# Kernel optimization log

Measured on AMD Instinct MI355X. Metric: run time of the kernel, lower is better.

## Reference

```python
import jax, jax.numpy as jnp
import numpy as np

N_NODES = 100000
N_EDGES = 3200000
N_GRAPHS = 256
HID = 128


def _glorot(key, shape):
    fan_in = shape[1]
    return jax.random.normal(key, shape, dtype=jnp.float32) / jnp.sqrt(jnp.float32(fan_in))


def setup_inputs() -> dict:
    key = jax.random.key(0)
    ks = jax.random.split(key, 16)
    x = jax.random.normal(ks[0], (N_NODES, 50), dtype=jnp.float32)
    edge_index = jax.random.randint(ks[1], (2, N_EDGES), 0, N_NODES, dtype=jnp.int32)
    batch = jnp.sort(jax.random.randint(ks[2], (N_NODES,), 0, N_GRAPHS, dtype=jnp.int32))
    d1, d2, d3 = HID, HID * 2, HID * 4
    params = {
        'w1l': _glorot(ks[3], (d1, 50)), 'b1': jnp.zeros((d1,), jnp.float32), 'w1r': _glorot(ks[4], (d1, 50)),
        'w2l': _glorot(ks[5], (d2, d1)), 'b2': jnp.zeros((d2,), jnp.float32), 'w2r': _glorot(ks[6], (d2, d1)),
        'w3l': _glorot(ks[7], (d3, d2)), 'b3': jnp.zeros((d3,), jnp.float32), 'w3r': _glorot(ks[8], (d3, d2)),
        'fc1_w': _glorot(ks[9], (d2, d3)), 'fc1_b': jnp.zeros((d2,), jnp.float32),
        'fc2_w': _glorot(ks[10], (d1, d2)), 'fc2_b': jnp.zeros((d1,), jnp.float32),
        'cls_w': _glorot(ks[11], (15, d1)), 'cls_b': jnp.zeros((15,), jnp.float32),
    }
    return {'x': x, 'edge_index': edge_index, 'batch': batch, **params}


def _sage_conv(x, src, dst, wl, b, wr):
    # PyG SAGEConv (mean aggr): out = lin_l(mean_j x_j) + lin_r(x_i)
    agg = jax.ops.segment_sum(x[src], dst, num_segments=N_NODES)
    deg = jax.ops.segment_sum(jnp.ones((src.shape[0],), x.dtype), dst, num_segments=N_NODES)
    agg = agg / jnp.maximum(deg, 1.0)[:, None]
    return agg @ wl.T + b + x @ wr.T


def reference(x, edge_index, batch,
              w1l, b1, w1r, w2l, b2, w2r, w3l, b3, w3r,
              fc1_w, fc1_b, fc2_w, fc2_b, cls_w, cls_b):
    src, dst = edge_index[0], edge_index[1]
    # eval mode: dropout is identity
    h = jax.nn.leaky_relu(_sage_conv(x, src, dst, w1l, b1, w1r), negative_slope=0.01)
    h = jax.nn.relu(_sage_conv(h, src, dst, w2l, b2, w2r))
    h = jax.nn.relu(_sage_conv(h, src, dst, w3l, b3, w3r))
    # global mean pool over graphs
    pooled = jax.ops.segment_sum(h, batch, num_segments=N_GRAPHS)
    cnt = jax.ops.segment_sum(jnp.ones((h.shape[0],), h.dtype), batch, num_segments=N_GRAPHS)
    pooled = pooled / jnp.maximum(cnt, 1.0)[:, None]
    z = jax.nn.relu(pooled @ fc1_w.T + fc1_b)
    z = jax.nn.relu(z @ fc2_w.T + fc2_b)
    return z @ cls_w.T + cls_b
```

## Files before the change

kernel.cpp:

```cpp
#include <hip/hip_runtime.h>
#include <hip/hip_bf16.h>

#define N_NODES 100000
#define N_EDGES 3200000
#define N_GRAPHS 256
#define CAP 80

typedef __hip_bfloat16 bf16;
using f32x4  = __attribute__((ext_vector_type(4))) float;
using f32x2  = __attribute__((ext_vector_type(2))) float;
using short8 = __attribute__((ext_vector_type(8))) short;

__global__ void rank_kernel(const int* __restrict__ dst, int* __restrict__ cnt,
                            unsigned short* __restrict__ rank) {
    int e = blockIdx.x * blockDim.x + threadIdx.x;
    if (e < N_EDGES) rank[e] = (unsigned short)atomicAdd(&cnt[dst[e]], 1);
}

__global__ void place_slot_kernel(const int* __restrict__ src, const int* __restrict__ dst,
                                  const unsigned short* __restrict__ rank,
                                  int* __restrict__ cols) {
    int e = blockIdx.x * blockDim.x + threadIdx.x;
    if (e < N_EDGES) {
        int r = rank[e];
        if (r < CAP) cols[dst[e] * CAP + r] = src[e];
    }
}

__global__ void invdeg_kernel(const int* __restrict__ cnt, float* __restrict__ invdeg) {
    int n = blockIdx.x * blockDim.x + threadIdx.x;
    if (n < N_NODES) invdeg[n] = 1.0f / fmaxf((float)cnt[n], 1.0f);
}

__global__ void xprep_kernel(const float* __restrict__ x, bf16* __restrict__ xb) {
    int t = blockIdx.x * blockDim.x + threadIdx.x;
    if (t >= N_NODES * 64) return;
    int n = t >> 6, f = t & 63;
    xb[t] = __float2bfloat16(f < 50 ? x[(size_t)n * 50 + f] : 0.f);
}

__device__ __forceinline__ void wcvt(const float* __restrict__ s, bf16* __restrict__ d,
                                     int Din, int Kp, int lt) {
    int o = lt / Kp, kk = lt % Kp;
    d[lt] = __float2bfloat16(kk < Din ? s[(size_t)o * Din + kk] : 0.f);
}

__global__ void wprep_all_kernel(const float* w1l, const float* w1r,
                                 const float* w2l, const float* w2r,
                                 const float* w3l, const float* w3r,
                                 bf16* w1l_b, bf16* w1r_b, bf16* w2l_b, bf16* w2r_b,
                                 bf16* w3l_b, bf16* w3r_b) {
    int t = blockIdx.x * blockDim.x + threadIdx.x;
    if      (t < 8192)   wcvt(w1l, w1l_b, 50, 64, t);
    else if (t < 16384)  wcvt(w1r, w1r_b, 50, 64, t - 8192);
    else if (t < 49152)  wcvt(w2l, w2l_b, 128, 128, t - 16384);
    else if (t < 81920)  wcvt(w2r, w2r_b, 128, 128, t - 49152);
    else if (t < 212992) wcvt(w3l, w3l_b, 256, 256, t - 81920);
    else if (t < 344064) wcvt(w3r, w3r_b, 256, 256, t - 212992);
}

template <int D>
__global__ void aggv_kernel(const bf16* __restrict__ h, const int* __restrict__ cnt,
                            const int* __restrict__ cols, const float* __restrict__ invdeg,
                            bf16* __restrict__ AG) {
    constexpr int L = D / 8;
    int n = blockIdx.x * (256 / L) + threadIdx.x / L;
    int lane = threadIdx.x % L;
    if (n >= N_NODES) return;
    const int* cp = cols + (size_t)n * CAP;
    int deg = min(cnt[n], CAP);
    float acc[8] = {};
    auto accum = [&](uint4 v) {
        const unsigned short* u = (const unsigned short*)&v;
#pragma unroll
        for (int i = 0; i < 8; ++i) {
            union { unsigned int ui; float f; } cv;
            cv.ui = ((unsigned int)u[i]) << 16;
            acc[i] += cv.f;
        }
    };
    int j = 0;
    for (; j + 4 <= deg; j += 4) {
        int c0 = cp[j], c1 = cp[j + 1], c2 = cp[j + 2], c3 = cp[j + 3];
        uint4 v0 = *(const uint4*)&h[(size_t)c0 * D + lane * 8];
        uint4 v1 = *(const uint4*)&h[(size_t)c1 * D + lane * 8];
        uint4 v2 = *(const uint4*)&h[(size_t)c2 * D + lane * 8];
        uint4 v3 = *(const uint4*)&h[(size_t)c3 * D + lane * 8];
        accum(v0); accum(v1); accum(v2); accum(v3);
    }
    for (; j < deg; ++j) accum(*(const uint4*)&h[(size_t)cp[j] * D + lane * 8]);
    float inv = invdeg[n];
    union { uint4 u; bf16 h8[8]; } o;
#pragma unroll
    for (int i = 0; i < 8; ++i) o.h8[i] = __float2bfloat16(acc[i] * inv);
    *(uint4*)&AG[(size_t)n * D + lane * 8] = o.u;
}

template <int D>
__global__ void aggv8_kernel(const unsigned char* __restrict__ h8,
                             const int* __restrict__ cnt,
                             const int* __restrict__ cols, const float* __restrict__ invdeg,
                             bf16* __restrict__ AG) {
    constexpr int L = D / 8;
    int n = blockIdx.x * (256 / L) + threadIdx.x / L;
    int lane = threadIdx.x % L;
    if (n >= N_NODES) return;
    const int* cp = cols + (size_t)n * CAP;
    int deg = min(cnt[n], CAP);
    float acc[8] = {};
    auto accum = [&](uint2 v) {
        f32x2 a0 = __builtin_amdgcn_cvt_pk_f32_fp8(v.x, false);
        f32x2 a1 = __builtin_amdgcn_cvt_pk_f32_fp8(v.x, true);
        f32x2 a2 = __builtin_amdgcn_cvt_pk_f32_fp8(v.y, false);
        f32x2 a3 = __builtin_amdgcn_cvt_pk_f32_fp8(v.y, true);
        acc[0] += a0[0]; acc[1] += a0[1]; acc[2] += a1[0]; acc[3] += a1[1];
        acc[4] += a2[0]; acc[5] += a2[1]; acc[6] += a3[0]; acc[7] += a3[1];
    };
    int j = 0;
    for (; j + 8 <= deg; j += 8) {
        uint2 v[8];
#pragma unroll
        for (int q = 0; q < 8; ++q)
            v[q] = *(const uint2*)&h8[(size_t)cp[j + q] * D + lane * 8];
#pragma unroll
        for (int q = 0; q < 8; ++q) accum(v[q]);
    }
    for (; j < deg; ++j) accum(*(const uint2*)&h8[(size_t)cp[j] * D + lane * 8]);
    float inv = invdeg[n];
    union { uint4 u; bf16 hb[8]; } o;
#pragma unroll
    for (int i = 0; i < 8; ++i) o.hb[i] = __float2bfloat16(acc[i] * inv);
    *(uint4*)&AG[(size_t)n * D + lane * 8] = o.u;
}

template <int ACT, int POOL, int OUT8>
__global__ __launch_bounds__(256) void glds_gemm(
        const bf16* __restrict__ A1, const bf16* __restrict__ A2, int Kh,
        const bf16* __restrict__ B1, const bf16* __restrict__ B2,
        const float* __restrict__ bias, bf16* __restrict__ out,
        unsigned char* __restrict__ out8,
        int M, int Dout,
        const int* __restrict__ batch, float* __restrict__ pooled) {
    __shared__ alignas(16) bf16 As[2][128][32];
    __shared__ alignas(16) bf16 Bs[2][128][32];
    __shared__ int sbatch[128];

    const int tid = threadIdx.x;
    const int n0 = blockIdx.y * 128;
    const int o0 = blockIdx.x * 128;

    if (POOL && tid < 128) {
        int n = n0 + tid;
        sbatch[tid] = (n < M) ? batch[n] : -1;
    }

    const int lane = tid & 63;
    const int w = tid >> 6;
    const int wr = w >> 1, wc = w & 1;
    const int lr = lane & 15, hi = lane >> 4;
    const int l4 = lane >> 2;
    const int kc8 = (lane & 3) * 8;

    f32x4 acc[4][4] = {};

    auto stage = [&](int buf, int k0) {
        const bf16* Ap;
        const bf16* Bp;
        int kk;
        if (k0 < Kh) { Ap = A1; Bp = B1; kk = k0; }
        else         { Ap = A2; Bp = B2; kk = k0 - Kh; }
#pragma unroll
        for (int c = 0; c < 2; ++c) {
            int rl = w * 32 + c * 16 + l4;
            size_t ga = (size_t)min(n0 + rl, M - 1) * (size_t)Kh + kk + kc8;
            __builtin_amdgcn_global_load_lds(
                (const __attribute__((address_space(1))) void*)(Ap + ga),
                (__attribute__((address_space(3))) void*)&As[buf][w * 32 + c * 16][0], 16, 0, 0);
            size_t gb = (size_t)(o0 + rl) * (size_t)Kh + kk + kc8;
            __builtin_amdgcn_global_load_lds(
                (const __attribute__((address_space(1))) void*)(Bp + gb),
                (__attribute__((address_space(3))) void*)&Bs[buf][w * 32 + c * 16][0], 16, 0, 0);
        }
    };

    const int nt = (2 * Kh) / 32;
    stage(0, 0);
    asm volatile("s_waitcnt vmcnt(0)\n\ts_barrier" ::: "memory");

    int cur = 0;
    for (int t = 0; t < nt; ++t) {
        if (t + 1 < nt) stage(cur ^ 1, (t + 1) * 32);

        short8 af[4], bfr[4];
#pragma unroll
        for (int m = 0; m < 4; ++m)
            af[m] = *(const short8*)&As[cur][wr * 64 + m * 16 + lr][hi * 8];
#pragma unroll
        for (int n = 0; n < 4; ++n)
            bfr[n] = *(const short8*)&Bs[cur][wc * 64 + n * 16 + lr][hi * 8];
#pragma unroll
        for (int m = 0; m < 4; ++m)
#pragma unroll
            for (int n = 0; n < 4; ++n)
                acc[m][n] = __builtin_amdgcn_mfma_f32_16x16x32_bf16(af[m], bfr[n], acc[m][n], 0, 0, 0);

        if (t + 1 < nt)
            asm volatile("s_waitcnt vmcnt(0)\n\ts_barrier" ::: "memory");
        cur ^= 1;
    }

    float bias_v[4];
#pragma unroll
    for (int n = 0; n < 4; ++n) bias_v[n] = bias[o0 + wc * 64 + n * 16 + lr];

    if (!POOL) {
#pragma unroll
        for (int m = 0; m < 4; ++m) {
#pragma unroll
            for (int j = 0; j < 4; ++j) {
                int row = n0 + wr * 64 + m * 16 + hi * 4 + j;
                if (row < M) {
#pragma unroll
                    for (int n = 0; n < 4; ++n) {
                        int col = o0 + wc * 64 + n * 16 + lr;
                        float s = acc[m][n][j] + bias_v[n];
                        if (ACT == 0) s = (s >= 0.f) ? s : 0.01f * s;
                        else          s = fmaxf(s, 0.f);
                        out[(size_t)row * Dout + col] = __float2bfloat16(s);
                        if (OUT8) {
                            int p = __builtin_amdgcn_cvt_pk_fp8_f32(s, s, 0, false);
                            out8[(size_t)row * Dout + col] = (unsigned char)(p & 0xff);
                        }
                    }
                }
            }
        }
    } else {
        int lastv = min(127, M - 1 - n0);
        int gmin = sbatch[0], gmax = sbatch[lastv];
        for (int g = gmin; g <= gmax; ++g) {
            float s[4] = {0.f, 0.f, 0.f, 0.f};
#pragma unroll
            for (int m = 0; m < 4; ++m) {
#pragma unroll
                for (int j = 0; j < 4; ++j) {
                    int rl = wr * 64 + m * 16 + hi * 4 + j;
                    if (sbatch[rl] == g) {
#pragma unroll
                        for (int n = 0; n < 4; ++n)
                            s[n] += fmaxf(acc[m][n][j] + bias_v[n], 0.f);
                    }
                }
            }
#pragma unroll
            for (int n = 0; n < 4; ++n) {
                float v = s[n];
                v += __shfl_xor(v, 16, 64);
                v += __shfl_xor(v, 32, 64);
                if (hi == 0)
                    atomicAdd(&pooled[(size_t)g * 512 + o0 + wc * 64 + n * 16 + lr], v);
            }
        }
    }
}

__global__ void bounds_kernel(const int* __restrict__ batch, int* __restrict__ gstart) {
    int g = blockIdx.x * blockDim.x + threadIdx.x;
    if (g > N_GRAPHS) return;
    int lo = 0, hi = N_NODES;
    while (lo < hi) {
        int mid = (lo + hi) >> 1;
        if (batch[mid] < g) lo = mid + 1;
        else hi = mid;
    }
    gstart[g] = lo;
}

__global__ void pool_finalize(float* __restrict__ pooled, const int* __restrict__ gstart) {
    int g = blockIdx.x;
    int f = threadIdx.x;
    float cnt = fmaxf((float)(gstart[g + 1] - gstart[g]), 1.0f);
    pooled[(size_t)g * 512 + f] /= cnt;
}

template <int ACT>
__global__ void mlp_kernel(const float* __restrict__ in, const float* __restrict__ w,
                           const float* __restrict__ b, float* __restrict__ out,
                           int M, int K, int O) {
    int t = blockIdx.x * blockDim.x + threadIdx.x;
    if (t >= M * O) return;
    int m = t / O, o = t % O;
    const float* ip = in + (size_t)m * K;
    const float* wp = w + (size_t)o * K;
    float s = 0.f;
    for (int k = 0; k < K; ++k) s += ip[k] * wp[k];
    s += b[o];
    if (ACT) s = fmaxf(s, 0.f);
    out[(size_t)m * O + o] = s;
}

extern "C" void kernel_launch(void* const* d_in, const int* in_sizes, int n_in,
                              void* d_out, int out_size, void* d_ws, size_t ws_size,
                              hipStream_t stream) {
    const float* x     = (const float*)d_in[0];
    const int*   ei    = (const int*)d_in[1];
    const int*   batch = (const int*)d_in[2];
    const float* w1l = (const float*)d_in[3];
    const float* b1  = (const float*)d_in[4];
    const float* w1r = (const float*)d_in[5];
    const float* w2l = (const float*)d_in[6];
    const float* b2  = (const float*)d_in[7];
    const float* w2r = (const float*)d_in[8];
    const float* w3l = (const float*)d_in[9];
    const float* b3  = (const float*)d_in[10];
    const float* w3r = (const float*)d_in[11];
    const float* fc1_w = (const float*)d_in[12];
    const float* fc1_b = (const float*)d_in[13];
    const float* fc2_w = (const float*)d_in[14];
    const float* fc2_b = (const float*)d_in[15];
    const float* cls_w = (const float*)d_in[16];
    const float* cls_b = (const float*)d_in[17];
    float* out = (float*)d_out;

    const int* src = ei;
    const int* dst = ei + N_EDGES;

    char* wsp = (char*)d_ws;
    size_t used = 0;
    auto alloc = [&](size_t bytes) {
        char* p = wsp + used;
        used += (bytes + 255) & ~(size_t)255;
        return p;
    };
    int*   cnt    = (int*)alloc((size_t)N_NODES * 4);
    int*   cols   = (int*)alloc((size_t)N_NODES * CAP * 4);
    float* invdeg = (float*)alloc((size_t)N_NODES * 4);
    int*   gstart = (int*)alloc((size_t)(N_GRAPHS + 1) * 4);
    bf16*  xb     = (bf16*)alloc((size_t)N_NODES * 64 * 2);
    char*  R      = alloc((size_t)N_NODES * 256 * 2);
    bf16*  AG     = (bf16*)R;
    bf16*  h1     = (bf16*)(R + (size_t)N_NODES * 128 * 2);
    bf16*  h2     = (bf16*)alloc((size_t)N_NODES * 256 * 2);
    unsigned short* rank = (unsigned short*)h2;
    unsigned char* h1_8 = (unsigned char*)alloc((size_t)N_NODES * 128);
    unsigned char* h2_8 = (unsigned char*)alloc((size_t)N_NODES * 256);
    bf16*  w1l_b  = (bf16*)alloc(128 * 64 * 2);
    bf16*  w1r_b  = (bf16*)alloc(128 * 64 * 2);
    bf16*  w2l_b  = (bf16*)alloc(256 * 128 * 2);
    bf16*  w2r_b  = (bf16*)alloc(256 * 128 * 2);
    bf16*  w3l_b  = (bf16*)alloc(512 * 256 * 2);
    bf16*  w3r_b  = (bf16*)alloc(512 * 256 * 2);
    float* pooled = (float*)alloc((size_t)N_GRAPHS * 512 * 4);
    float* z1     = (float*)alloc((size_t)N_GRAPHS * 256 * 4);
    float* z2     = (float*)alloc((size_t)N_GRAPHS * 128 * 4);

    if (ws_size < used) return;

    hipMemsetAsync(cnt, 0, (size_t)N_NODES * 4, stream);
    rank_kernel<<<(N_EDGES + 255) / 256, 256, 0, stream>>>(dst, cnt, rank);
    place_slot_kernel<<<(N_EDGES + 255) / 256, 256, 0, stream>>>(src, dst, rank, cols);
    invdeg_kernel<<<(N_NODES + 255) / 256, 256, 0, stream>>>(cnt, invdeg);
    bounds_kernel<<<2, 160, 0, stream>>>(batch, gstart);

    xprep_kernel<<<(N_NODES * 64 + 255) / 256, 256, 0, stream>>>(x, xb);
    wprep_all_kernel<<<(344064 + 255) / 256, 256, 0, stream>>>(
        w1l, w1r, w2l, w2r, w3l, w3r, w1l_b, w1r_b, w2l_b, w2r_b, w3l_b, w3r_b);

    const int MB = (N_NODES + 127) / 128;

    aggv_kernel<64><<<(N_NODES * 8 + 255) / 256, 256, 0, stream>>>(xb, cnt, cols, invdeg, AG);
    glds_gemm<0, 0, 1><<<dim3(1, MB), 256, 0, stream>>>(
        AG, xb, 64, w1l_b, w1r_b, b1, h1, h1_8, N_NODES, 128, nullptr, nullptr);

    aggv8_kernel<128><<<(N_NODES * 16 + 255) / 256, 256, 0, stream>>>(
        h1_8, cnt, cols, invdeg, AG);
    glds_gemm<1, 0, 1><<<dim3(2, MB), 256, 0, stream>>>(
        AG, h1, 128, w2l_b, w2r_b, b2, h2, h2_8, N_NODES, 256, nullptr, nullptr);

    aggv8_kernel<256><<<(N_NODES * 32 + 255) / 256, 256, 0, stream>>>(
        h2_8, cnt, cols, invdeg, AG);
    hipMemsetAsync(pooled, 0, (size_t)N_GRAPHS * 512 * 4, stream);
    glds_gemm<1, 1, 0><<<dim3(4, MB), 256, 0, stream>>>(
        AG, h2, 256, w3l_b, w3r_b, b3, nullptr, nullptr, N_NODES, 512, batch, pooled);
    pool_finalize<<<N_GRAPHS, 512, 0, stream>>>(pooled, gstart);

    mlp_kernel<1><<<(N_GRAPHS * 256 + 255) / 256, 256, 0, stream>>>(
        pooled, fc1_w, fc1_b, z1, N_GRAPHS, 512, 256);
    mlp_kernel<1><<<(N_GRAPHS * 128 + 255) / 256, 256, 0, stream>>>(
        z1, fc2_w, fc2_b, z2, N_GRAPHS, 256, 128);
    mlp_kernel<0><<<(N_GRAPHS * 15 + 255) / 256, 256, 0, stream>>>(
        z2, cls_w, cls_b, out, N_GRAPHS, 128, 15);
}
```

Baseline: 698.7 us.

## Build padded adjacency via two-level bucket sort with shared-memory atomics

Replaces the global-atomic rank/place graph build with a multi-pass bucketed counting sort. Edges are histogrammed by 64-node bucket in shared memory, prefix-scanned, scattered into a packed edge buffer, and then placed into per-node slots with shared-memory atomics. The aim is to remove 3.2M contended global atomics and the random scattered writes, and to fuse the invdeg computation. In exchange it adds six kernel launches, a serial single-block scan, and reuses the h1_8 and h2 buffers as scratch.

```diff
diff --git a/kernel.cpp b/kernel.cpp
--- a/kernel.cpp
+++ b/kernel.cpp
@@ -5,31 +5,125 @@
 #define N_EDGES 3200000
 #define N_GRAPHS 256
 #define CAP 80
+#define NB 1563
+#define NPB 64
+#define PBLK 512
+#define EPB 6250
 
 typedef __hip_bfloat16 bf16;
 using f32x4  = __attribute__((ext_vector_type(4))) float;
 using f32x2  = __attribute__((ext_vector_type(2))) float;
 using short8 = __attribute__((ext_vector_type(8))) short;
 
-__global__ void rank_kernel(const int* __restrict__ dst, int* __restrict__ cnt,
-                            unsigned short* __restrict__ rank) {
-    int e = blockIdx.x * blockDim.x + threadIdx.x;
-    if (e < N_EDGES) rank[e] = (unsigned short)atomicAdd(&cnt[dst[e]], 1);
-}
-
-__global__ void place_slot_kernel(const int* __restrict__ src, const int* __restrict__ dst,
-                                  const unsigned short* __restrict__ rank,
-                                  int* __restrict__ cols) {
-    int e = blockIdx.x * blockDim.x + threadIdx.x;
-    if (e < N_EDGES) {
-        int r = rank[e];
-        if (r < CAP) cols[dst[e] * CAP + r] = src[e];
-    }
-}
-
-__global__ void invdeg_kernel(const int* __restrict__ cnt, float* __restrict__ invdeg) {
-    int n = blockIdx.x * blockDim.x + threadIdx.x;
-    if (n < N_NODES) invdeg[n] = 1.0f / fmaxf((float)cnt[n], 1.0f);
+__global__ __launch_bounds__(256) void p1_count(const int* __restrict__ dst,
+                                                int* __restrict__ bcount) {
+    __shared__ int hist[NB];
+    int i = blockIdx.x;
+    for (int b = threadIdx.x; b < NB; b += 256) hist[b] = 0;
+    __syncthreads();
+    int base = i * EPB;
+    for (int j = threadIdx.x; j < EPB; j += 256)
+        atomicAdd(&hist[dst[base + j] >> 6], 1);
+    __syncthreads();
+    for (int b = threadIdx.x; b < NB; b += 256) bcount[(size_t)b * PBLK + i] = hist[b];
+}
+
+__global__ __launch_bounds__(512) void p2a_total(const int* __restrict__ bcount,
+                                                 int* __restrict__ btotal) {
+    __shared__ int red[512];
+    int b = blockIdx.x;
+    red[threadIdx.x] = bcount[(size_t)b * PBLK + threadIdx.x];
+    __syncthreads();
+    for (int off = 256; off > 0; off >>= 1) {
+        if (threadIdx.x < off) red[threadIdx.x] += red[threadIdx.x + off];
+        __syncthreads();
+    }
+    if (threadIdx.x == 0) btotal[b] = red[0];
+}
+
+__global__ __launch_bounds__(1024) void p2b_scan(const int* __restrict__ btotal,
+                                                 int* __restrict__ bbase) {
+    __shared__ int buf[1024];
+    __shared__ int carry;
+    if (threadIdx.x == 0) carry = 0;
+    __syncthreads();
+    for (int t = 0; t < NB; t += 1024) {
+        int i = t + threadIdx.x;
+        int v = (i < NB) ? btotal[i] : 0;
+        buf[threadIdx.x] = v;
+        __syncthreads();
+        for (int off = 1; off < 1024; off <<= 1) {
+            int tv = (threadIdx.x >= off) ? buf[threadIdx.x - off] : 0;
+            __syncthreads();
+            buf[threadIdx.x] += tv;
+            __syncthreads();
+        }
+        if (i < NB) bbase[i] = carry + buf[threadIdx.x] - v;
+        __syncthreads();
+        if (threadIdx.x == 0) carry += buf[1023];
+        __syncthreads();
+    }
+    if (threadIdx.x == 0) bbase[NB] = carry;
+}
+
+__global__ __launch_bounds__(512) void p2c_off(const int* __restrict__ bcount,
+                                               const int* __restrict__ bbase,
+                                               int* __restrict__ off) {
+    __shared__ int buf[512];
+    int b = blockIdx.x;
+    int v = bcount[(size_t)b * PBLK + threadIdx.x];
+    buf[threadIdx.x] = v;
+    __syncthreads();
+    for (int o = 1; o < 512; o <<= 1) {
+        int t = (threadIdx.x >= o) ? buf[threadIdx.x - o] : 0;
+        __syncthreads();
+        buf[threadIdx.x] += t;
+        __syncthreads();
+    }
+    off[(size_t)threadIdx.x * NB + b] = bbase[b] + buf[threadIdx.x] - v;
+}
+
+__global__ __launch_bounds__(256) void p3_scatter(const int* __restrict__ src,
+                                                  const int* __restrict__ dst,
+                                                  const int* __restrict__ off,
+                                                  unsigned int* __restrict__ ebuf) {
+    __shared__ int loff[NB];
+    int i = blockIdx.x;
+    for (int b = threadIdx.x; b < NB; b += 256) loff[b] = off[(size_t)i * NB + b];
+    __syncthreads();
+    int base = i * EPB;
+    for (int j = threadIdx.x; j < EPB; j += 256) {
+        int d = dst[base + j];
+        int p = atomicAdd(&loff[d >> 6], 1);
+        ebuf[p] = ((unsigned)src[base + j] << 6) | (unsigned)(d & 63);
+    }
+}
+
+__global__ __launch_bounds__(256) void p4_csr(const unsigned int* __restrict__ ebuf,
+                                              const int* __restrict__ bbase,
+                                              int* __restrict__ cols, int* __restrict__ cnt,
+                                              float* __restrict__ invdeg) {
+    __shared__ int lcnt[NPB];
+    int b = blockIdx.x;
+    if (threadIdx.x < NPB) lcnt[threadIdx.x] = 0;
+    __syncthreads();
+    int s = bbase[b], e = bbase[b + 1];
+    int n0 = b * NPB;
+    for (int j = s + threadIdx.x; j < e; j += 256) {
+        unsigned int p = ebuf[j];
+        int dl = p & 63;
+        int r = atomicAdd(&lcnt[dl], 1);
+        if (r < CAP) cols[(size_t)(n0 + dl) * CAP + r] = (int)(p >> 6);
+    }
+    __syncthreads();
+    if (threadIdx.x < NPB) {
+        int n = n0 + threadIdx.x;
+        if (n < N_NODES) {
+            int c = lcnt[threadIdx.x];
+            cnt[n] = c;
+            invdeg[n] = 1.0f / fmaxf((float)c, 1.0f);
+        }
+    }
 }
 
 __global__ void xprep_kernel(const float* __restrict__ x, bf16* __restrict__ xb) {
@@ -341,7 +435,6 @@
     bf16*  AG     = (bf16*)R;
     bf16*  h1     = (bf16*)(R + (size_t)N_NODES * 128 * 2);
     bf16*  h2     = (bf16*)alloc((size_t)N_NODES * 256 * 2);
-    unsigned short* rank = (unsigned short*)h2;
     unsigned char* h1_8 = (unsigned char*)alloc((size_t)N_NODES * 128);
     unsigned char* h2_8 = (unsigned char*)alloc((size_t)N_NODES * 256);
     bf16*  w1l_b  = (bf16*)alloc(128 * 64 * 2);
@@ -354,12 +447,20 @@
     float* z1     = (float*)alloc((size_t)N_GRAPHS * 256 * 4);
     float* z2     = (float*)alloc((size_t)N_GRAPHS * 128 * 4);
 
+    int* bcount = (int*)h1_8;
+    int* btotal = bcount + (size_t)NB * PBLK;
+    int* bbase  = btotal + NB;
+    int* off    = bbase + NB + 1;
+    unsigned int* ebuf = (unsigned int*)h2;
+
     if (ws_size < used) return;
 
-    hipMemsetAsync(cnt, 0, (size_t)N_NODES * 4, stream);
-    rank_kernel<<<(N_EDGES + 255) / 256, 256, 0, stream>>>(dst, cnt, rank);
-    place_slot_kernel<<<(N_EDGES + 255) / 256, 256, 0, stream>>>(src, dst, rank, cols);
-    invdeg_kernel<<<(N_NODES + 255) / 256, 256, 0, stream>>>(cnt, invdeg);
+    p1_count<<<PBLK, 256, 0, stream>>>(dst, bcount);
+    p2a_total<<<NB, 512, 0, stream>>>(bcount, btotal);
+    p2b_scan<<<1, 1024, 0, stream>>>(btotal, bbase);
+    p2c_off<<<NB, 512, 0, stream>>>(bcount, bbase, off);
+    p3_scatter<<<PBLK, 256, 0, stream>>>(src, dst, off, ebuf);
+    p4_csr<<<NB, 256, 0, stream>>>(ebuf, bbase, cols, cnt, invdeg);
     bounds_kernel<<<2, 160, 0, stream>>>(batch, gstart);
 
     xprep_kernel<<<(N_NODES * 64 + 255) / 256, 256, 0, stream>>>(x, xb);
```

Result: faster. 612.0 us (-12.4%).
